# Kernel optimization log

Hardware: AMD Instinct MI355X
Metric: run time of the kernel (lower is better)

The kernel has to match this reference:

```python
import jax, jax.numpy as jnp
import numpy as np

N, C, K, KEIG, B, NG, H = 32768, 128, 5, 128, 64, 512, 4
E = 524288
EPS = 1e-5


def setup_inputs() -> dict:
    key = jax.random.key(0)
    ks = iter(jax.random.split(key, 40))
    def nrm(shape, scale):
        return jax.random.normal(next(ks), shape, jnp.float32) * scale
    s = 1.0 / np.sqrt(C)
    return dict(
        x=nrm((N, C), 1.0),
        U=nrm((N, KEIG), 1.0 / np.sqrt(N)),
        Lambda=jax.random.uniform(next(ks), (KEIG,), jnp.float32, 0.0, 2.0),
        lambda_max=jnp.full((1,), 2.0, jnp.float32),
        w_spa1=nrm((C, C), s), b_spa1=jnp.zeros((C,), jnp.float32),
        w_spa2=nrm((C, C), s), b_spa2=jnp.zeros((C,), jnp.float32),
        w_spe1=nrm((C, C), s), b_spe1=jnp.zeros((C,), jnp.float32),
        w_spe2=nrm((C, C), s), b_spe2=jnp.zeros((C,), jnp.float32),
        cheb_w=nrm((K, C, C), s), cheb_b=jnp.zeros((C,), jnp.float32),
        gamma=jnp.ones((1,), jnp.float32),
        w_proj=nrm((C, C), s),
        w_qkv=nrm((C, 3 * C), s), b_qkv=jnp.zeros((3 * C,), jnp.float32),
        w_out=nrm((C, C), s), b_out=jnp.zeros((C,), jnp.float32),
        mlp_w1=nrm((C, 2 * C), s), mlp_b1=jnp.zeros((2 * C,), jnp.float32),
        mlp_w2=nrm((2 * C, C), 1.0 / np.sqrt(2 * C)), mlp_b2=jnp.zeros((C,), jnp.float32),
        bn1_w=jnp.ones((C,), jnp.float32), bn1_b=jnp.zeros((C,), jnp.float32),
        bn2_w=jnp.ones((C,), jnp.float32), bn2_b=jnp.zeros((C,), jnp.float32),
        bn3_w=jnp.ones((C,), jnp.float32), bn3_b=jnp.zeros((C,), jnp.float32),
        edge_index=jax.random.randint(next(ks), (2, E), 0, N, jnp.int64) if jax.config.jax_enable_x64 else jax.random.randint(next(ks), (2, E), 0, N, jnp.int32),
        batch=jnp.repeat(jnp.arange(B), NG),  # 64 graphs of 512 nodes each
    )


def _mlp2(h, w1, b1, w2, b2):
    return jnp.maximum(h @ w1 + b1, 0.0) @ w2 + b2


def _bn(h, w, b):
    # train-mode BatchNorm1d over node dim (biased variance), GPSConv default norm
    mu = h.mean(0)
    var = jnp.mean((h - mu) ** 2, 0)
    return (h - mu) * jax.lax.rsqrt(var + EPS) * w + b


def _cheb(x, src, dst, lam, Ws, bias):
    # L_hat = (2/lambda_max) * (I - D^{-1/2} A D^{-1/2}) - I ; sym normalization
    deg = jax.ops.segment_sum(jnp.ones_like(src, x.dtype), src, num_segments=N)
    dis = jnp.where(deg > 0, 1.0 / jnp.sqrt(deg), 0.0)
    w = dis[src] * dis[dst]  # [E]
    scale = 2.0 / lam
    def lhat(v):
        agg = jax.ops.segment_sum(w[:, None] * v[src], dst, num_segments=N)
        return (scale - 1.0) * v - scale * agg
    Tx0 = x
    out = Tx0 @ Ws[0]
    Tx1 = lhat(Tx0)
    out = out + Tx1 @ Ws[1]
    for k in range(2, K):
        Tx2 = 2.0 * lhat(Tx1) - Tx0
        out = out + Tx2 @ Ws[k]
        Tx0, Tx1 = Tx1, Tx2
    return out + bias


def _mha(xd, w_qkv, b_qkv, w_out, b_out):
    Bq, n, _ = xd.shape
    dh = C // H
    qkv = xd @ w_qkv + b_qkv  # [B,n,3C]
    q, k, v = jnp.split(qkv, 3, axis=-1)
    heads = lambda t: t.reshape(Bq, n, H, dh).transpose(0, 2, 1, 3)
    q, k, v = heads(q), heads(k), heads(v)
    a = jax.nn.softmax(jnp.einsum('bhqd,bhkd->bhqk', q, k) / np.sqrt(dh), axis=-1)
    o = jnp.einsum('bhqk,bhkd->bhqd', a, v).transpose(0, 2, 1, 3).reshape(Bq, n, C)
    return o @ w_out + b_out


def reference(x, U, Lambda, lambda_max,
              w_spa1, b_spa1, w_spa2, b_spa2,
              w_spe1, b_spe1, w_spe2, b_spe2,
              cheb_w, cheb_b, gamma, w_proj,
              w_qkv, b_qkv, w_out, b_out,
              mlp_w1, mlp_b1, mlp_w2, mlp_b2,
              bn1_w, bn1_b, bn2_w, bn2_b, bn3_w, bn3_b,
              edge_index, batch):
    src, dst = edge_index[0], edge_index[1]
    lam = lambda_max[0]
    # ---- SpectralLocalNN (GPSConv local conv branch) ----
    x_sp = _mlp2(x, w_spa1, b_spa1, w_spa2, b_spa2)
    out_local = _cheb(x_sp, src, dst, lam, cheb_w, cheb_b)
    x_spec = _mlp2(x, w_spe1, b_spe1, w_spe2, b_spe2)
    h_proj = x_spec @ w_proj
    s_lam = jnp.exp(-gamma[0] * Lambda ** 2)  # [k_eig]
    out_spectral = U @ (s_lam[:, None] * (U.T @ h_proj))
    h1 = _bn(out_local + out_spectral + x, bn1_w, bn1_b)
    # ---- global attention branch (equal-size graphs -> dense reshape) ----
    xd = x.reshape(B, NG, C)
    h2 = _mha(xd, w_qkv, b_qkv, w_out, b_out).reshape(N, C)
    h2 = _bn(h2 + x, bn2_w, bn2_b)
    # ---- combine + MLP ----
    out = h1 + h2
    out = out + _mlp2(out, mlp_w1, mlp_b1, mlp_w2, mlp_b2)
    return _bn(out, bn3_w, bn3_b)
```

## Files before the change

### kernel.cpp

```cpp
#include <hip/hip_runtime.h>

typedef short bf16x8 __attribute__((ext_vector_type(8)));
typedef short bf16x4 __attribute__((ext_vector_type(4)));
typedef float f32x4 __attribute__((ext_vector_type(4)));

#define DEVI __device__ __forceinline__

constexpr int N   = 32768;
constexpr int C   = 128;
constexpr int E   = 524288;
constexpr float EPSV = 1e-5f;
constexpr int UT_BLOCKS = 128;
constexpr int HB  = 64;
constexpr int EPB = E / HB;
constexpr float QSCALE = 0.17677669529663687f * 1.4426950408889634f;

DEVI float bf2f(ushort u){ return __uint_as_float(((uint)u) << 16); }
DEVI ushort f2bf(float f){
  uint u = __float_as_uint(f);
  return (ushort)((u + 0x7fffu + ((u >> 16) & 1u)) >> 16);
}
DEVI uint cvtpk(float lo, float hi){
  uint r;
  asm("v_cvt_pk_bf16_f32 %0, %1, %2" : "=v"(r) : "v"(lo), "v"(hi));
  return r;
}
DEVI float fexp2(float x){
  float r;
  asm("v_exp_f32 %0, %1" : "=v"(r) : "v"(x));
  return r;
}
DEVI float sane(float v){ if (!(v == v)) return 0.f; return fminf(fmaxf(v, -1e30f), 1e30f); }
DEVI bool mode_fp32(const uint* lmraw){ return (lmraw[0] & 0xffffu) == 0u; }

constexpr int CSZ[28] = {128,1,16384,128,16384,128,16384,128,16384,128,81920,128,
                         1,16384,49152,384,16384,128,32768,256,32768,128,
                         128,128,128,128,128,128};
constexpr int COF[28] = {0,128,192,16576,16704,33088,33216,49600,49728,66112,
                         66240,148160,148288,148352,164736,213888,214272,230656,
                         230784,263552,263808,296576,296704,296832,296960,297088,
                         297216,297344};
constexpr int CAN_SMALL_TOTAL = 297472;

constexpr int WT_SPA1 = 0;
constexpr int WT_SPA2 = 16384;
constexpr int WT_SPE1 = 32768;
constexpr int WT_SPE2 = 49152;
constexpr int WT_PROJ = 65536;
constexpr int WT_CHEB = 81920;
constexpr int WT_QKV  = 163840;
constexpr int WT_WOUT = 212992;
constexpr int WT_MLP1 = 229376;
constexpr int WT_MLP2 = 262144;
constexpr int WT_TOTAL = 294912;

struct CvtArgs { const void* src[28]; };

DEVI ushort cvt_elem(const void* p, int j, bool f32){
  return f32 ? f2bf(((const float*)p)[j]) : ((const ushort*)p)[j];
}

__global__ __launch_bounds__(256) void prep_all(CvtArgs a,
    const void* __restrict__ xs, const void* __restrict__ Us,
    ushort* __restrict__ canx, ushort* __restrict__ canu,
    ushort* __restrict__ cs, ushort* __restrict__ wt,
    int* __restrict__ zp, const uint* __restrict__ lmraw)
{
  bool f32 = mode_fp32(lmraw);
  int b = blockIdx.x, tid = threadIdx.x;
  if (b < 8192) {
    size_t e = ((size_t)b * 256 + tid) * 4;
    bool isU = e >= (size_t)N * C;
    size_t off = isU ? e - (size_t)N * C : e;
    const void* src = isU ? Us : xs;
    ushort* dst = isU ? canu : canx;
    ushort4 o;
    if (f32) {
      float4 v = *(const float4*)((const float*)src + off);
      o.x = f2bf(v.x); o.y = f2bf(v.y); o.z = f2bf(v.z); o.w = f2bf(v.w);
    } else {
      o = *(const ushort4*)((const ushort*)src + off);
    }
    *(ushort4*)(dst + off) = o;
  } else if (b < 9354) {
    int idx = (b - 8192) * 256 + tid;
    #pragma unroll 1
    for (int s = 0; s < 28; s++) {
      if (idx < CSZ[s]) { cs[COF[s] + idx] = cvt_elem(a.src[s], idx, f32); return; }
      idx -= CSZ[s];
    }
  } else if (b < 10506) {
    int i = (b - 9354) * 256 + tid;
    if (i < 81920) {
      int m = i >> 14, r = i & 16383; int k = r >> 7, n = r & 127;
      const void* src = m==0?a.src[2] : m==1?a.src[4] : m==2?a.src[6] : m==3?a.src[8] : a.src[13];
      wt[m*16384 + n*128 + k] = cvt_elem(src, r, f32);
    } else if (i < 163840) {
      int j = i - 81920; int m = j >> 14, r = j & 16383; int k = r >> 7, n = r & 127;
      wt[WT_CHEB + n*640 + m*128 + k] = cvt_elem(a.src[10], j, f32);
    } else if (i < 212992) {
      int j = i - 163840; int k = j / 384, n = j % 384;
      wt[WT_QKV + n*128 + k] = cvt_elem(a.src[14], j, f32);
    } else if (i < 229376) {
      int j = i - 212992; int k = j >> 7, n = j & 127;
      wt[WT_WOUT + n*128 + k] = cvt_elem(a.src[16], j, f32);
    } else if (i < 262144) {
      int j = i - 229376; int k = j >> 8, n = j & 255;
      wt[WT_MLP1 + n*128 + k] = cvt_elem(a.src[18], j, f32);
    } else if (i < WT_TOTAL) {
      int j = i - 262144; int k = j >> 7, n = j & 127;
      wt[WT_MLP2 + n*256 + k] = cvt_elem(a.src[20], j, f32);
    }
  } else {
    int i = (b - 10506) * 256 + tid;
    if (i < 6144) zp[i] = 0;
  }
}

__global__ __launch_bounds__(1024) void hist_lds(const int* __restrict__ ei,
    int* __restrict__ cei, ushort* __restrict__ part)
{
  __shared__ uint hist[N / 2];
  int t = threadIdx.x;
  int b = blockIdx.x;
  bool i64 = ((ei[1] | ei[3] | ei[5] | ei[7]) == 0);
  size_t j0 = (size_t)b * EPB;
  #pragma unroll
  for (int i = t; i < N / 2; i += 1024) hist[i] = 0u;
  __syncthreads();
  for (int k = t; k < EPB; k += 1024) {
    size_t j = j0 + k;
    int v = (i64 ? ei[2 * j] : ei[j]) & (N - 1);
    cei[j] = v;
    atomicAdd(&hist[v >> 1], 1u << ((v & 1) * 16));
  }
  __syncthreads();
  uint* po = (uint*)(part + (size_t)b * N);
  for (int i = t; i < N / 2; i += 1024) po[i] = hist[i];
}

__global__ __launch_bounds__(256) void reduce_cnt(const ushort* __restrict__ part,
    int* __restrict__ cdt, float* __restrict__ dis)
{
  int d = blockIdx.x * 256 + threadIdx.x;
  int s = 0, tt = 0;
  #pragma unroll 8
  for (int b = 0; b < HB; b++) s  += part[(size_t)b * N + d];
  #pragma unroll 8
  for (int b = 0; b < HB; b++) tt += part[(size_t)(HB + b) * N + d];
  cdt[d] = tt;
  dis[d] = s > 0 ? rsqrtf((float)s) : 0.f;
}

__global__ __launch_bounds__(1024) void scan_kernel(const int* __restrict__ cnt,
                                                    int* __restrict__ row_ptr)
{
  __shared__ int sums[1024];
  int t = threadIdx.x;
  int loc[32]; int s = 0;
  int base = t * 32;
  #pragma unroll
  for (int i = 0; i < 32; i++) { loc[i] = s; s += cnt[base + i]; }
  sums[t] = s;
  __syncthreads();
  for (int off = 1; off < 1024; off <<= 1) {
    int v = (t >= off) ? sums[t - off] : 0;
    __syncthreads();
    sums[t] += v;
    __syncthreads();
  }
  int pre = (t == 0) ? 0 : sums[t - 1];
  #pragma unroll
  for (int i = 0; i < 32; i++) row_ptr[base + i] = pre + loc[i];
}

__global__ __launch_bounds__(256) void off_kernel(const int* __restrict__ rp,
    const ushort* __restrict__ part, int* __restrict__ off2)
{
  int d = blockIdx.x * 256 + threadIdx.x;
  int run = rp[d];
  #pragma unroll 8
  for (int b = 0; b < HB; b++) {
    off2[(size_t)b * N + d] = run;
    run += part[(size_t)(HB + b) * N + d];
  }
}

__global__ __launch_bounds__(1024) void edge_scatter(const int* __restrict__ cei,
    const int* __restrict__ off2, const float* __restrict__ dis,
    int2* __restrict__ ep)
{
  __shared__ int base[N];
  int t = threadIdx.x;
  int b = blockIdx.x;
  for (int i = t; i < N; i += 1024) base[i] = off2[(size_t)b * N + i];
  __syncthreads();
  size_t e0 = (size_t)b * EPB;
  for (int k = t; k < EPB; k += 1024) {
    size_t e = e0 + k;
    int s = cei[e], d = cei[e + E];
    int slot = atomicAdd(&base[d], 1);
    int2 v; v.x = s; v.y = __float_as_int(dis[s] * dis[d]);
    ep[slot] = v;
  }
}

template<int K, int COLS, bool RELU, int OMODE, bool BIAS, bool RES, int ASTR, int OSTR, bool QSC, bool STATS>
__global__ __launch_bounds__(256) void gemm_lds(
    const ushort* __restrict__ A, const ushort* __restrict__ WT,
    const ushort* __restrict__ bias, const ushort* __restrict__ res,
    void* __restrict__ outp, float* __restrict__ gstats)
{
  constexpr int NSEG = COLS / 128;
  constexpr int NKC = K / 128;
  constexpr int BP = 136;
  __shared__ ushort Bs[128 * BP];
  __shared__ float ls[STATS ? 256 : 1];
  int tid = threadIdx.x;
  int lane = tid & 63, wave = tid >> 6;
  int quad = lane >> 4, l16 = lane & 15;
  int seg = (NSEG > 1) ? (blockIdx.x % NSEG) : 0;
  int rb  = (NSEG > 1) ? (blockIdx.x / NSEG) : blockIdx.x;
  int row0 = rb * 64 + wave * 16;
  const ushort* wseg = WT + (size_t)(seg * 128) * K;

  f32x4 acc[8];
  #pragma unroll
  for (int nt = 0; nt < 8; nt++) acc[nt] = (f32x4){0.f, 0.f, 0.f, 0.f};

  for (int kc = 0; kc < NKC; kc++) {
    if (kc) __syncthreads();
    #pragma unroll
    for (int i = tid; i < 2048; i += 256) {
      int col = i >> 4, ko = (i & 15) * 8;
      *(bf16x8*)&Bs[col * BP + ko] =
          *(const bf16x8*)(wseg + (size_t)col * K + kc * 128 + ko);
    }
    __syncthreads();
    bf16x8 a[4];
    const ushort* ap = A + (size_t)(row0 + l16) * ASTR + kc * 128 + quad * 8;
    #pragma unroll
    for (int kk = 0; kk < 4; kk++) a[kk] = *(const bf16x8*)(ap + kk * 32);
    #pragma unroll
    for (int kk = 0; kk < 4; kk++) {
      #pragma unroll
      for (int nt = 0; nt < 8; nt++) {
        bf16x8 b = *(const bf16x8*)(&Bs[(nt * 16 + l16) * BP + kk * 32 + quad * 8]);
        acc[nt] = __builtin_amdgcn_mfma_f32_16x16x32_bf16(a[kk], b, acc[nt], 0, 0, 0);
      }
    }
  }

  if (STATS) {
    if (tid < 256) ls[tid] = 0.f;
    __syncthreads();
  }

  #pragma unroll
  for (int nt = 0; nt < 8; nt++) {
    int col = seg * 128 + nt * 16 + l16;
    float bv = 0.f;
    if (BIAS) bv = bf2f(bias[col]);
    float cs_ = 0.f, cs2 = 0.f;
    #pragma unroll
    for (int r = 0; r < 4; r++) {
      int row = row0 + quad * 4 + r;
      size_t oi = (size_t)row * OSTR + col;
      float v = acc[nt][r] + bv;
      if (RES) v += bf2f(res[(size_t)row * COLS + col]);
      if (RELU) v = fmaxf(v, 0.f);
      if (QSC && col < 128) v *= QSCALE;
      float nv;
      if (OMODE == 0)      { ((ushort*)outp)[oi] = f2bf(v); nv = v; }
      else if (OMODE == 1) { ((float*)outp)[oi] = v; nv = v; }
      else                 { float* fo = (float*)outp + oi; nv = *fo + v; *fo = nv; }
      if (STATS) { float sv = sane(nv); cs_ += sv; cs2 += sv * sv; }
    }
    if (STATS) { atomicAdd(&ls[col], cs_); atomicAdd(&ls[128 + col], cs2); }
  }

  if (STATS) {
    __syncthreads();
    float* gs = gstats + (blockIdx.x & 7) * 256;
    if (tid < 128) {
      atomicAdd(&gs[tid], ls[tid]);
      atomicAdd(&gs[128 + tid], ls[128 + tid]);
    }
  }
}

template<bool THIRD, int OSTR>
__global__ __launch_bounds__(256) void gemm_chain(
    const ushort* __restrict__ A,
    const ushort* __restrict__ W1, const ushort* __restrict__ B1,
    const ushort* __restrict__ W2, const ushort* __restrict__ B2,
    const ushort* __restrict__ W3,
    ushort* __restrict__ outp)
{
  constexpr int BP = 136;
  __shared__ ushort Bs[128 * BP];
  __shared__ ushort Ts[64 * BP];
  int tid = threadIdx.x;
  int lane = tid & 63, wave = tid >> 6;
  int quad = lane >> 4, l16 = lane & 15;
  int row0 = blockIdx.x * 64 + wave * 16;
  int lw = wave * 16;

  for (int i = tid; i < 2048; i += 256) {
    int col = i >> 4, ko = (i & 15) * 8;
    *(bf16x8*)&Bs[col * BP + ko] = *(const bf16x8*)(W1 + (size_t)col * 128 + ko);
  }
  __syncthreads();
  bf16x8 a[4];
  {
    const ushort* ap = A + (size_t)(row0 + l16) * 128 + quad * 8;
    #pragma unroll
    for (int kk = 0; kk < 4; kk++) a[kk] = *(const bf16x8*)(ap + kk * 32);
  }
  f32x4 acc[8];
  #pragma unroll
  for (int nt = 0; nt < 8; nt++) acc[nt] = (f32x4){0.f, 0.f, 0.f, 0.f};
  #pragma unroll
  for (int kk = 0; kk < 4; kk++)
    #pragma unroll
    for (int nt = 0; nt < 8; nt++) {
      bf16x8 b = *(const bf16x8*)(&Bs[(nt * 16 + l16) * BP + kk * 32 + quad * 8]);
      acc[nt] = __builtin_amdgcn_mfma_f32_16x16x32_bf16(a[kk], b, acc[nt], 0, 0, 0);
    }
  #pragma unroll
  for (int nt = 0; nt < 8; nt++) {
    int col = nt * 16 + l16;
    float bv = bf2f(B1[col]);
    #pragma unroll
    for (int r = 0; r < 4; r++)
      Ts[(lw + quad * 4 + r) * BP + col] = f2bf(fmaxf(acc[nt][r] + bv, 0.f));
  }
  __syncthreads();

  for (int i = tid; i < 2048; i += 256) {
    int col = i >> 4, ko = (i & 15) * 8;
    *(bf16x8*)&Bs[col * BP + ko] = *(const bf16x8*)(W2 + (size_t)col * 128 + ko);
  }
  #pragma unroll
  for (int kk = 0; kk < 4; kk++)
    a[kk] = *(const bf16x8*)(&Ts[(lw + l16) * BP + kk * 32 + quad * 8]);
  __syncthreads();
  #pragma unroll
  for (int nt = 0; nt < 8; nt++) acc[nt] = (f32x4){0.f, 0.f, 0.f, 0.f};
  #pragma unroll
  for (int kk = 0; kk < 4; kk++)
    #pragma unroll
    for (int nt = 0; nt < 8; nt++) {
      bf16x8 b = *(const bf16x8*)(&Bs[(nt * 16 + l16) * BP + kk * 32 + quad * 8]);
      acc[nt] = __builtin_amdgcn_mfma_f32_16x16x32_bf16(a[kk], b, acc[nt], 0, 0, 0);
    }

  if (!THIRD) {
    #pragma unroll
    for (int nt = 0; nt < 8; nt++) {
      int col = nt * 16 + l16;
      float bv = bf2f(B2[col]);
      #pragma unroll
      for (int r = 0; r < 4; r++)
        outp[(size_t)(row0 + quad * 4 + r) * OSTR + col] = f2bf(acc[nt][r] + bv);
    }
    return;
  }

  __syncthreads();
  #pragma unroll
  for (int nt = 0; nt < 8; nt++) {
    int col = nt * 16 + l16;
    float bv = bf2f(B2[col]);
    #pragma unroll
    for (int r = 0; r < 4; r++)
      Ts[(lw + quad * 4 + r) * BP + col] = f2bf(acc[nt][r] + bv);
  }
  __syncthreads();
  for (int i = tid; i < 2048; i += 256) {
    int col = i >> 4, ko = (i & 15) * 8;
    *(bf16x8*)&Bs[col * BP + ko] = *(const bf16x8*)(W3 + (size_t)col * 128 + ko);
  }
  #pragma unroll
  for (int kk = 0; kk < 4; kk++)
    a[kk] = *(const bf16x8*)(&Ts[(lw + l16) * BP + kk * 32 + quad * 8]);
  __syncthreads();
  #pragma unroll
  for (int nt = 0; nt < 8; nt++) acc[nt] = (f32x4){0.f, 0.f, 0.f, 0.f};
  #pragma unroll
  for (int kk = 0; kk < 4; kk++)
    #pragma unroll
    for (int nt = 0; nt < 8; nt++) {
      bf16x8 b = *(const bf16x8*)(&Bs[(nt * 16 + l16) * BP + kk * 32 + quad * 8]);
      acc[nt] = __builtin_amdgcn_mfma_f32_16x16x32_bf16(a[kk], b, acc[nt], 0, 0, 0);
    }
  #pragma unroll
  for (int nt = 0; nt < 8; nt++) {
    int col = nt * 16 + l16;
    #pragma unroll
    for (int r = 0; r < 4; r++)
      outp[(size_t)(row0 + quad * 4 + r) * OSTR + col] = f2bf(acc[nt][r]);
  }
}

__global__ __launch_bounds__(256) void gemm_mlp(
    const ushort* __restrict__ A,
    const ushort* __restrict__ W1, const ushort* __restrict__ B1,
    const ushort* __restrict__ W2, const ushort* __restrict__ B2,
    const ushort* __restrict__ res, float* __restrict__ outp,
    float* __restrict__ gstats)
{
  constexpr int BP = 136;
  constexpr int HP = 264;
  __shared__ ushort Bs[128 * BP];
  __shared__ ushort Hs[64 * HP];
  __shared__ float ls[256];
  int tid = threadIdx.x;
  int lane = tid & 63, wave = tid >> 6;
  int quad = lane >> 4, l16 = lane & 15;
  int row0 = blockIdx.x * 64 + wave * 16;
  int lw = wave * 16;

  bf16x8 a[4];
  {
    const ushort* ap = A + (size_t)(row0 + l16) * 128 + quad * 8;
    #pragma unroll
    for (int kk = 0; kk < 4; kk++) a[kk] = *(const bf16x8*)(ap + kk * 32);
  }

  for (int seg = 0; seg < 2; seg++) {
    if (seg) __syncthreads();
    for (int i = tid; i < 2048; i += 256) {
      int col = i >> 4, ko = (i & 15) * 8;
      *(bf16x8*)&Bs[col * BP + ko] =
          *(const bf16x8*)(W1 + (size_t)(seg * 128 + col) * 128 + ko);
    }
    __syncthreads();
    f32x4 acc[8];
    #pragma unroll
    for (int nt = 0; nt < 8; nt++) acc[nt] = (f32x4){0.f, 0.f, 0.f, 0.f};
    #pragma unroll
    for (int kk = 0; kk < 4; kk++)
      #pragma unroll
      for (int nt = 0; nt < 8; nt++) {
        bf16x8 b = *(const bf16x8*)(&Bs[(nt * 16 + l16) * BP + kk * 32 + quad * 8]);
        acc[nt] = __builtin_amdgcn_mfma_f32_16x16x32_bf16(a[kk], b, acc[nt], 0, 0, 0);
      }
    #pragma unroll
    for (int nt = 0; nt < 8; nt++) {
      int col = seg * 128 + nt * 16 + l16;
      float bv = bf2f(B1[col]);
      #pragma unroll
      for (int r = 0; r < 4; r++)
        Hs[(lw + quad * 4 + r) * HP + col] = f2bf(fmaxf(acc[nt][r] + bv, 0.f));
    }
  }
  __syncthreads();
  if (tid < 256) ls[tid] = 0.f;

  f32x4 acc2[8];
  #pragma unroll
  for (int nt = 0; nt < 8; nt++) acc2[nt] = (f32x4){0.f, 0.f, 0.f, 0.f};
  for (int kc = 0; kc < 2; kc++) {
    if (kc) __syncthreads();
    for (int i = tid; i < 2048; i += 256) {
      int col = i >> 4, ko = (i & 15) * 8;
      *(bf16x8*)&Bs[col * BP + ko] =
          *(const bf16x8*)(W2 + (size_t)col * 256 + kc * 128 + ko);
    }
    bf16x8 a2[4];
    #pragma unroll
    for (int kk = 0; kk < 4; kk++)
      a2[kk] = *(const bf16x8*)(&Hs[(lw + l16) * HP + kc * 128 + kk * 32 + quad * 8]);
    __syncthreads();
    #pragma unroll
    for (int kk = 0; kk < 4; kk++)
      #pragma unroll
      for (int nt = 0; nt < 8; nt++) {
        bf16x8 b = *(const bf16x8*)(&Bs[(nt * 16 + l16) * BP + kk * 32 + quad * 8]);
        acc2[nt] = __builtin_amdgcn_mfma_f32_16x16x32_bf16(a2[kk], b, acc2[nt], 0, 0, 0);
      }
  }

  #pragma unroll
  for (int nt = 0; nt < 8; nt++) {
    int col = nt * 16 + l16;
    float bv = bf2f(B2[col]);
    float cs_ = 0.f, cs2 = 0.f;
    #pragma unroll
    for (int r = 0; r < 4; r++) {
      int row = row0 + quad * 4 + r;
      float v = acc2[nt][r] + bv + bf2f(res[(size_t)row * 128 + col]);
      outp[(size_t)row * 128 + col] = v;
      float sv = sane(v); cs_ += sv; cs2 += sv * sv;
    }
    atomicAdd(&ls[col], cs_); atomicAdd(&ls[128 + col], cs2);
  }
  __syncthreads();
  float* gs = gstats + (blockIdx.x & 7) * 256;
  if (tid < 128) {
    atomicAdd(&gs[tid], ls[tid]);
    atomicAdd(&gs[128 + tid], ls[128 + tid]);
  }
}

__global__ __launch_bounds__(256) void spmm_cheb(
    const int* __restrict__ row_ptr, const int2* __restrict__ ep,
    const ushort* __restrict__ v,
    const ushort* __restrict__ txprev, ushort* __restrict__ txout,
    const ushort* __restrict__ lambda_max, int first, int str)
{
  int wave = threadIdx.x >> 6, lane = threadIdx.x & 63;
  int sub = lane >> 4, l16 = lane & 15;
  int d = blockIdx.x * 4 + wave;
  float lm = bf2f(lambda_max[0]);
  float scale = 2.f / lm;
  if (!(scale == scale) || fabsf(scale) > 1e6f) scale = 1.f;
  int beg = row_ptr[d];
  int end = (d == N - 1) ? E : row_ptr[d + 1];
  float acc[8] = {0.f,0.f,0.f,0.f,0.f,0.f,0.f,0.f};
  int j0 = beg + sub;
  int2 e2 = ep[j0 < end ? j0 : 0];
  for (int jb = beg; jb < end; jb += 4) {
    int jn = jb + 4 + sub;
    int2 en = ep[jn < end ? jn : 0];
    bool ok = (jb + sub) < end;
    int s = e2.x & (N - 1);
    float w = ok ? __int_as_float(e2.y) : 0.f;
    bf16x8 vv = *(const bf16x8*)(v + (size_t)s * str + l16 * 8);
    #pragma unroll
    for (int i = 0; i < 8; i++) acc[i] += w * bf2f((ushort)vv[i]);
    e2 = en;
  }
  #pragma unroll
  for (int i = 0; i < 8; i++) {
    acc[i] += __shfl_xor(acc[i], 16);
    acc[i] += __shfl_xor(acc[i], 32);
  }
  if (sub == 0) {
    bf16x8 vd = *(const bf16x8*)(v + (size_t)d * str + l16 * 8);
    bf16x8 tp;
    if (!first) tp = *(const bf16x8*)(txprev + (size_t)d * str + l16 * 8);
    bf16x8 ov;
    #pragma unroll
    for (int i = 0; i < 8; i++) {
      float r = (scale - 1.f) * bf2f((ushort)vd[i]) - scale * acc[i];
      if (!first) r = 2.f * r - bf2f((ushort)tp[i]);
      ov[i] = (short)f2bf(r);
    }
    *(bf16x8*)(txout + (size_t)d * str + l16 * 8) = ov;
  }
}

__global__ __launch_bounds__(256) void ut_mfma(const ushort* __restrict__ U,
    const ushort* __restrict__ hp, float* __restrict__ parts)
{
  constexpr int RP = 40;
  __shared__ ushort Ut[128 * RP];
  __shared__ ushort Ht[128 * RP];
  int t = threadIdx.x;
  int lane = t & 63, wave = t >> 6;
  int quad = lane >> 4, l16 = lane & 15;

  f32x4 acc[2][8];
  #pragma unroll
  for (int a = 0; a < 2; a++)
    #pragma unroll
    for (int ct = 0; ct < 8; ct++) acc[a][ct] = (f32x4){0.f, 0.f, 0.f, 0.f};

  for (int ch = 0; ch < 8; ch++) {
    int n0 = blockIdx.x * 256 + ch * 32;
    __syncthreads();
    for (int i = t; i < 2048; i += 256) {
      int r2 = i >> 7, c = i & 127;
      uint u0 = U [(size_t)(n0 + r2 * 2) * 128 + c];
      uint u1 = U [(size_t)(n0 + r2 * 2 + 1) * 128 + c];
      *(uint*)&Ut[c * RP + r2 * 2] = (u0 & 0xffffu) | (u1 << 16);
      uint h0 = hp[(size_t)(n0 + r2 * 2) * 128 + c];
      uint h1 = hp[(size_t)(n0 + r2 * 2 + 1) * 128 + c];
      *(uint*)&Ht[c * RP + r2 * 2] = (h0 & 0xffffu) | (h1 << 16);
    }
    __syncthreads();
    bf16x8 bfr[8];
    #pragma unroll
    for (int ct = 0; ct < 8; ct++)
      bfr[ct] = *(const bf16x8*)(&Ht[(ct * 16 + l16) * RP + quad * 8]);
    #pragma unroll
    for (int a = 0; a < 2; a++) {
      int kt = wave * 2 + a;
      bf16x8 af = *(const bf16x8*)(&Ut[(kt * 16 + l16) * RP + quad * 8]);
      #pragma unroll
      for (int ct = 0; ct < 8; ct++)
        acc[a][ct] = __builtin_amdgcn_mfma_f32_16x16x32_bf16(af, bfr[ct], acc[a][ct], 0, 0, 0);
    }
  }

  float* po = parts + (size_t)blockIdx.x * 16384;
  #pragma unroll
  for (int a = 0; a < 2; a++) {
    int kt = wave * 2 + a;
    #pragma unroll
    for (int ct = 0; ct < 8; ct++)
      #pragma unroll
      for (int r = 0; r < 4; r++)
        po[(kt * 16 + quad * 4 + r) * 128 + ct * 16 + l16] = acc[a][ct][r];
  }
}

__global__ __launch_bounds__(256) void reduce_mt(const float* __restrict__ parts,
    const ushort* __restrict__ Lambda, const ushort* __restrict__ gamma,
    ushort* __restrict__ MT)
{
  int e = blockIdx.x * 256 + threadIdx.x;
  int keig = e >> 7, c = e & 127;
  float s = 0.f;
  for (int p = 0; p < UT_BLOCKS; p++) s += parts[(size_t)p * 16384 + e];
  float g = bf2f(gamma[0]);
  float lam = bf2f(Lambda[keig]);
  float sl = __expf(-g * lam * lam);
  MT[c * 128 + keig] = f2bf(sl * s);
}

__global__ __launch_bounds__(256) void bn_apply(const float* __restrict__ h,
    const float* __restrict__ st, const ushort* __restrict__ gw,
    const ushort* __restrict__ gb, const ushort* __restrict__ add,
    void* __restrict__ out, const uint* __restrict__ lmraw, int final_out)
{
  __shared__ float sk[128], sb[128];
  int tid = threadIdx.x;
  if (tid < 128) {
    float s = 0.f, s2 = 0.f;
    #pragma unroll
    for (int rr = 0; rr < 8; rr++) {
      s  += st[rr * 256 + tid];
      s2 += st[rr * 256 + 128 + tid];
    }
    float mu  = s * (1.f / 32768.f);
    float var = fmaxf(s2 * (1.f / 32768.f) - mu * mu, 0.f);
    float k = rsqrtf(var + EPSV) * bf2f(gw[tid]);
    sk[tid] = k;
    sb[tid] = bf2f(gb[tid]) - mu * k;
  }
  __syncthreads();
  size_t e = ((size_t)blockIdx.x * 256 + tid) * 4;
  int c0 = (int)(e & 127);
  float4 hv = *(const float4*)(h + e);
  float xv[4] = {sane(hv.x), sane(hv.y), sane(hv.z), sane(hv.w)};
  float addv[4] = {0.f, 0.f, 0.f, 0.f};
  if (add) {
    ushort4 av = *(const ushort4*)(add + e);
    addv[0] = bf2f(av.x); addv[1] = bf2f(av.y);
    addv[2] = bf2f(av.z); addv[3] = bf2f(av.w);
  }
  float r[4];
  #pragma unroll
  for (int j = 0; j < 4; j++) {
    int c = c0 + j;
    r[j] = xv[j] * sk[c] + sb[c] + addv[j];
  }
  if (final_out && mode_fp32(lmraw)) {
    float4 o4; o4.x = r[0]; o4.y = r[1]; o4.z = r[2]; o4.w = r[3];
    *(float4*)((float*)out + e) = o4;
  } else {
    ushort4 o;
    o.x = f2bf(r[0]); o.y = f2bf(r[1]); o.z = f2bf(r[2]); o.w = f2bf(r[3]);
    *(ushort4*)((ushort*)out + e) = o;
  }
}

__global__ __launch_bounds__(512) void attn_mfma(const ushort* __restrict__ qkv,
                                                 ushort* __restrict__ attn)
{
  constexpr int VP = 516;
  constexpr int KP = 40;
  __shared__ ushort Kt[512 * KP];
  __shared__ ushort Vt[32 * VP];
  int b = blockIdx.x;
  int g = b >> 3, hh = (b >> 1) & 3, half = b & 1;
  int lane = threadIdx.x & 63, wave = threadIdx.x >> 6;
  int quad = lane >> 4, l16 = lane & 15;
  const ushort* base = qkv + (size_t)g * 512 * 384;

  for (int i = threadIdx.x; i < 512 * 4; i += 512) {
    int key = i >> 2, c8 = (i & 3) * 8;
    *(bf16x8*)&Kt[key * KP + c8] =
        *(const bf16x8*)(base + (size_t)key * 384 + 128 + hh * 32 + c8);
  }
  for (int i = threadIdx.x; i < 256 * 8; i += 512) {
    int kp = i >> 3, d4 = (i & 7) * 4;
    const ushort* va = base + (size_t)(2 * kp) * 384 + 256 + hh * 32 + d4;
    ushort4 a = *(const ushort4*)va;
    ushort4 c = *(const ushort4*)(va + 384);
    *(uint*)&Vt[(d4 + 0) * VP + 2 * kp] = (uint)a.x | ((uint)c.x << 16);
    *(uint*)&Vt[(d4 + 1) * VP + 2 * kp] = (uint)a.y | ((uint)c.y << 16);
    *(uint*)&Vt[(d4 + 2) * VP + 2 * kp] = (uint)a.z | ((uint)c.z << 16);
    *(uint*)&Vt[(d4 + 3) * VP + 2 * kp] = (uint)a.w | ((uint)c.w << 16);
  }
  __syncthreads();

  int q0 = half * 256 + wave * 32;
  bf16x8 qf[2];
  #pragma unroll
  for (int i = 0; i < 2; i++)
    qf[i] = *(const bf16x8*)(base + (size_t)(q0 + i * 16 + l16) * 384 + hh * 32 + quad * 8);

  f32x4 O[2][2];
  #pragma unroll
  for (int dt = 0; dt < 2; dt++)
    #pragma unroll
    for (int i = 0; i < 2; i++) O[dt][i] = (f32x4){0.f, 0.f, 0.f, 0.f};
  float lsum[2] = {0.f, 0.f};

  union PU { uint u[4]; bf16x8 v; };
  union VU { uint2 a[2]; bf16x8 v; };

  for (int kt2 = 0; kt2 < 16; kt2++) {
    int k0 = kt2 * 32;
    bf16x8 kfA = *(const bf16x8*)&Kt[(k0 + l16) * KP + quad * 8];
    bf16x8 kfB = *(const bf16x8*)&Kt[(k0 + 16 + l16) * KP + quad * 8];
    PU pw[2];
    #pragma unroll
    for (int i = 0; i < 2; i++) {
      f32x4 sA = __builtin_amdgcn_mfma_f32_16x16x32_bf16(kfA, qf[i], (f32x4){0.f,0.f,0.f,0.f}, 0, 0, 0);
      f32x4 sB = __builtin_amdgcn_mfma_f32_16x16x32_bf16(kfB, qf[i], (f32x4){0.f,0.f,0.f,0.f}, 0, 0, 0);
      float p0 = fexp2(fminf(sA[0], 86.5f));
      float p1 = fexp2(fminf(sA[1], 86.5f));
      float p2 = fexp2(fminf(sA[2], 86.5f));
      float p3 = fexp2(fminf(sA[3], 86.5f));
      float p4 = fexp2(fminf(sB[0], 86.5f));
      float p5 = fexp2(fminf(sB[1], 86.5f));
      float p6 = fexp2(fminf(sB[2], 86.5f));
      float p7 = fexp2(fminf(sB[3], 86.5f));
      lsum[i] += ((p0 + p1) + (p2 + p3)) + ((p4 + p5) + (p6 + p7));
      pw[i].u[0] = cvtpk(p0, p1); pw[i].u[1] = cvtpk(p2, p3);
      pw[i].u[2] = cvtpk(p4, p5); pw[i].u[3] = cvtpk(p6, p7);
    }
    #pragma unroll
    for (int dt = 0; dt < 2; dt++) {
      int drow = (dt * 16 + l16) * VP;
      VU vu;
      vu.a[0] = *(const uint2*)&Vt[drow + k0 + quad * 4];
      vu.a[1] = *(const uint2*)&Vt[drow + k0 + 16 + quad * 4];
      #pragma unroll
      for (int i = 0; i < 2; i++)
        O[dt][i] = __builtin_amdgcn_mfma_f32_16x16x32_bf16(vu.v, pw[i].v, O[dt][i], 0, 0, 0);
    }
  }

  #pragma unroll
  for (int i = 0; i < 2; i++) {
    float l = lsum[i];
    l += __shfl_xor(l, 16);
    l += __shfl_xor(l, 32);
    lsum[i] = 1.f / l;
  }

  #pragma unroll
  for (int i = 0; i < 2; i++) {
    size_t node = (size_t)g * 512 + q0 + i * 16 + l16;
    #pragma unroll
    for (int dt = 0; dt < 2; dt++) {
      uint2 o;
      o.x = cvtpk(O[dt][i][0] * lsum[i], O[dt][i][1] * lsum[i]);
      o.y = cvtpk(O[dt][i][2] * lsum[i], O[dt][i][3] * lsum[i]);
      *(uint2*)(attn + node * 128 + hh * 32 + dt * 16 + quad * 4) = o;
    }
  }
}

constexpr size_t KB = 1024;
constexpr size_t MB = 1048576;
constexpr size_t OFF_WT    = 0;
constexpr size_t OFF_CDT   = 576 * KB;
constexpr size_t OFF_RP    = 704 * KB;
constexpr size_t OFF_DIS   = 832 * KB;
constexpr size_t OFF_MT    = 960 * KB;
constexpr size_t OFF_STATS = 1024 * KB;
constexpr size_t OFF_CEI   = 6  * MB;
constexpr size_t OFF_EP    = 10 * MB;
constexpr size_t OFF_CANX  = 14 * MB;
constexpr size_t OFF_CANU  = 22 * MB;
constexpr size_t OFF_CANS  = 30 * MB;
constexpr size_t OFF_F1    = 31 * MB;
constexpr size_t OFF_HPROJ = 39 * MB;
constexpr size_t OFF_TBIG  = 47 * MB;
constexpr size_t OFF_PARTH = OFF_TBIG;
constexpr size_t OFF_OFF2  = OFF_TBIG + 8 * MB;
constexpr size_t OFF_PARTS = 87 * MB;

extern "C" void kernel_launch(void* const* d_in, const int* in_sizes, int n_in,
                              void* d_out, int out_size, void* d_ws, size_t ws_size,
                              hipStream_t stream) {
  (void)in_sizes; (void)n_in; (void)out_size; (void)ws_size;
  const uint* lmraw = (const uint*)d_in[3];
  const int*  ei    = (const int*)d_in[30];

  char* W = (char*)d_ws;
  ushort* wt    = (ushort*)(W + OFF_WT);
  int*    cdt   = (int*)(W + OFF_CDT);
  int*    rp    = (int*)(W + OFF_RP);
  float*  dis   = (float*)(W + OFF_DIS);
  ushort* MT    = (ushort*)(W + OFF_MT);
  float*  stats = (float*)(W + OFF_STATS);
  int*    cei   = (int*)(W + OFF_CEI);
  int2*   ep    = (int2*)(W + OFF_EP);
  ushort* part  = (ushort*)(W + OFF_PARTH);
  int*    off2  = (int*)(W + OFF_OFF2);
  ushort* canx  = (ushort*)(W + OFF_CANX);
  ushort* canu  = (ushort*)(W + OFF_CANU);
  ushort* cs    = (ushort*)(W + OFF_CANS);
  float*  F1    = (float*)(W + OFF_F1);
  ushort* hproj = (ushort*)(W + OFF_HPROJ);
  ushort* Tbig  = (ushort*)(W + OFF_TBIG);
  ushort* qkvb  = (ushort*)(W + OFF_TBIG);
  float*  parts = (float*)(W + OFF_PARTS);
  ushort* attnb = (ushort*)(W + OFF_PARTS);
  ushort* h1    = (ushort*)(W + OFF_CANU);
  ushort* comb  = (ushort*)(W + OFF_CANX);

  const ushort* cLambda = cs + COF[0];
  const ushort* cLmx    = cs + COF[1];
  const ushort* cBspa1  = cs + COF[3];
  const ushort* cBspa2  = cs + COF[5];
  const ushort* cBspe1  = cs + COF[7];
  const ushort* cBspe2  = cs + COF[9];
  const ushort* cChebB  = cs + COF[11];
  const ushort* cGam    = cs + COF[12];
  const ushort* cBqkv   = cs + COF[15];
  const ushort* cBout   = cs + COF[17];
  const ushort* cMb1    = cs + COF[19];
  const ushort* cMb2    = cs + COF[21];
  const ushort* cBn1w   = cs + COF[22];
  const ushort* cBn1b   = cs + COF[23];
  const ushort* cBn2w   = cs + COF[24];
  const ushort* cBn2b   = cs + COF[25];
  const ushort* cBn3w   = cs + COF[26];
  const ushort* cBn3b   = cs + COF[27];

  const ushort* NUL = nullptr;
  float* NULF = nullptr;

  CvtArgs ca;
  ca.src[0]  = d_in[2];  ca.src[1]  = d_in[3];  ca.src[2]  = d_in[4];
  ca.src[3]  = d_in[5];  ca.src[4]  = d_in[6];  ca.src[5]  = d_in[7];
  ca.src[6]  = d_in[8];  ca.src[7]  = d_in[9];  ca.src[8]  = d_in[10];
  ca.src[9]  = d_in[11]; ca.src[10] = d_in[12]; ca.src[11] = d_in[13];
  ca.src[12] = d_in[14]; ca.src[13] = d_in[15]; ca.src[14] = d_in[16];
  ca.src[15] = d_in[17]; ca.src[16] = d_in[18]; ca.src[17] = d_in[19];
  ca.src[18] = d_in[20]; ca.src[19] = d_in[21]; ca.src[20] = d_in[22];
  ca.src[21] = d_in[23]; ca.src[22] = d_in[24]; ca.src[23] = d_in[25];
  ca.src[24] = d_in[26]; ca.src[25] = d_in[27]; ca.src[26] = d_in[28];
  ca.src[27] = d_in[29];
  prep_all<<<10530, 256, 0, stream>>>(ca, d_in[0], d_in[1], canx, canu, cs, wt,
                                      (int*)(W + OFF_STATS), lmraw);

  hist_lds<<<2 * HB, 1024, 0, stream>>>(ei, cei, part);
  reduce_cnt<<<N / 256, 256, 0, stream>>>(part, cdt, dis);
  scan_kernel<<<1, 1024, 0, stream>>>(cdt, rp);
  off_kernel<<<N / 256, 256, 0, stream>>>(rp, part, off2);
  edge_scatter<<<HB, 1024, 0, stream>>>(cei, off2, dis, ep);

  dim3 g1(512), g3(1536), bb(256);
  gemm_chain<false, 640><<<g1, bb, 0, stream>>>(canx, wt + WT_SPA1, cBspa1,
      wt + WT_SPA2, cBspa2, NUL, Tbig);
  gemm_chain<true, 128><<<g1, bb, 0, stream>>>(canx, wt + WT_SPE1, cBspe1,
      wt + WT_SPE2, cBspe2, wt + WT_PROJ, hproj);

  ut_mfma<<<UT_BLOCKS, 256, 0, stream>>>(canu, hproj, parts);
  reduce_mt<<<64, 256, 0, stream>>>(parts, cLambda, cGam, MT);

  spmm_cheb<<<N / 4, 256, 0, stream>>>(rp, ep, Tbig,       NUL,        Tbig + 128, cLmx, 1, 640);
  spmm_cheb<<<N / 4, 256, 0, stream>>>(rp, ep, Tbig + 128, Tbig,       Tbig + 256, cLmx, 0, 640);
  spmm_cheb<<<N / 4, 256, 0, stream>>>(rp, ep, Tbig + 256, Tbig + 128, Tbig + 384, cLmx, 0, 640);
  spmm_cheb<<<N / 4, 256, 0, stream>>>(rp, ep, Tbig + 384, Tbig + 256, Tbig + 512, cLmx, 0, 640);
  gemm_lds<640,128,false,1,true ,false,640,128,false,false><<<g1, bb, 0, stream>>>(Tbig, wt + WT_CHEB, cChebB, NUL, F1, NULF);

  gemm_lds<128,128,false,2,false,true ,128,128,false,true ><<<g1, bb, 0, stream>>>(canu, MT, NUL, canx, F1, stats);
  bn_apply<<<(N * C) / 1024, 256, 0, stream>>>(F1, stats, cBn1w, cBn1b, NUL, h1, lmraw, 0);

  gemm_lds<128,384,false,0,true ,false,128,384,true ,false><<<g3, bb, 0, stream>>>(canx, wt + WT_QKV, cBqkv, NUL, qkvb, NULF);
  attn_mfma<<<512, 512, 0, stream>>>(qkvb, attnb);
  gemm_lds<128,128,false,1,true ,true ,128,128,false,true ><<<g1, bb, 0, stream>>>(attnb, wt + WT_WOUT, cBout, canx, F1, stats + 2048);
  bn_apply<<<(N * C) / 1024, 256, 0, stream>>>(F1, stats + 2048, cBn2w, cBn2b, h1, comb, lmraw, 0);

  gemm_mlp<<<g1, bb, 0, stream>>>(comb, wt + WT_MLP1, cMb1, wt + WT_MLP2, cMb2, comb, F1, stats + 4096);
  bn_apply<<<(N * C) / 1024, 256, 0, stream>>>(F1, stats + 4096, cBn3w, cBn3b, NUL, d_out, lmraw, 1);
}
```

Measured before the change: 504.9 us.

## Fuse BN1/BN2 apply, add dedicated QKV GEMM, deepen SpMM prefetch

Merges the two separate BatchNorm apply passes into one kernel that reads both fp32 pre-norm buffers and writes the combined bf16 sum. This removes the write and re-read of the intermediate h1 buffer and one kernel launch, at the cost of a second fp32 buffer in the workspace. It also replaces the templated QKV GEMM with a kernel that keeps the A tile in registers and loops over the three 128-column weight segments. The Chebyshev SpMM now prefetches edges two iterations ahead and gathers the feature row one iteration ahead, to hide gather latency at the cost of extra registers.

```diff
diff --git a/kernel.cpp b/kernel.cpp
--- a/kernel.cpp
+++ b/kernel.cpp
@@ -289,6 +289,56 @@
   }
 }
 
+__global__ __launch_bounds__(256) void gemm_qkv(
+    const ushort* __restrict__ A, const ushort* __restrict__ WT,
+    const ushort* __restrict__ bias, ushort* __restrict__ outp)
+{
+  constexpr int BP = 136;
+  __shared__ ushort Bs[128 * BP];
+  int tid = threadIdx.x;
+  int lane = tid & 63, wave = tid >> 6;
+  int quad = lane >> 4, l16 = lane & 15;
+  int row0 = blockIdx.x * 64 + wave * 16;
+  bf16x8 a[4];
+  {
+    const ushort* ap = A + (size_t)(row0 + l16) * 128 + quad * 8;
+    #pragma unroll
+    for (int kk = 0; kk < 4; kk++) a[kk] = *(const bf16x8*)(ap + kk * 32);
+  }
+
+  #pragma unroll 1
+  for (int seg = 0; seg < 3; seg++) {
+    if (seg) __syncthreads();
+    for (int i = tid; i < 2048; i += 256) {
+      int col = i >> 4, ko = (i & 15) * 8;
+      *(bf16x8*)&Bs[col * BP + ko] =
+          *(const bf16x8*)(WT + (size_t)(seg * 128 + col) * 128 + ko);
+    }
+    __syncthreads();
+    f32x4 acc[8];
+    #pragma unroll
+    for (int nt = 0; nt < 8; nt++) acc[nt] = (f32x4){0.f, 0.f, 0.f, 0.f};
+    #pragma unroll
+    for (int kk = 0; kk < 4; kk++)
+      #pragma unroll
+      for (int nt = 0; nt < 8; nt++) {
+        bf16x8 b = *(const bf16x8*)(&Bs[(nt * 16 + l16) * BP + kk * 32 + quad * 8]);
+        acc[nt] = __builtin_amdgcn_mfma_f32_16x16x32_bf16(a[kk], b, acc[nt], 0, 0, 0);
+      }
+    #pragma unroll
+    for (int nt = 0; nt < 8; nt++) {
+      int col = seg * 128 + nt * 16 + l16;
+      float bv = bf2f(bias[col]);
+      #pragma unroll
+      for (int r = 0; r < 4; r++) {
+        float v = acc[nt][r] + bv;
+        if (seg == 0) v *= QSCALE;
+        outp[(size_t)(row0 + quad * 4 + r) * 384 + col] = f2bf(v);
+      }
+    }
+  }
+}
+
 template<bool THIRD, int OSTR>
 __global__ __launch_bounds__(256) void gemm_chain(
     const ushort* __restrict__ A,
@@ -520,17 +570,18 @@
   int end = (d == N - 1) ? E : row_ptr[d + 1];
   float acc[8] = {0.f,0.f,0.f,0.f,0.f,0.f,0.f,0.f};
   int j0 = beg + sub;
-  int2 e2 = ep[j0 < end ? j0 : 0];
+  int2 eA = ep[j0 < end ? j0 : 0];
+  int2 eB = ep[(j0 + 4) < end ? (j0 + 4) : 0];
+  bf16x8 vA = *(const bf16x8*)(v + (size_t)(eA.x & (N - 1)) * str + l16 * 8);
   for (int jb = beg; jb < end; jb += 4) {
-    int jn = jb + 4 + sub;
-    int2 en = ep[jn < end ? jn : 0];
+    int jc = jb + 8 + sub;
+    int2 eC = ep[jc < end ? jc : 0];
+    bf16x8 vB = *(const bf16x8*)(v + (size_t)(eB.x & (N - 1)) * str + l16 * 8);
     bool ok = (jb + sub) < end;
-    int s = e2.x & (N - 1);
-    float w = ok ? __int_as_float(e2.y) : 0.f;
-    bf16x8 vv = *(const bf16x8*)(v + (size_t)s * str + l16 * 8);
-    #pragma unroll
-    for (int i = 0; i < 8; i++) acc[i] += w * bf2f((ushort)vv[i]);
-    e2 = en;
+    float w = ok ? __int_as_float(eA.y) : 0.f;
+    #pragma unroll
+    for (int i = 0; i < 8; i++) acc[i] += w * bf2f((ushort)vA[i]);
+    eA = eB; eB = eC; vA = vB;
   }
   #pragma unroll
   for (int i = 0; i < 8; i++) {
@@ -666,6 +717,50 @@
     o.x = f2bf(r[0]); o.y = f2bf(r[1]); o.z = f2bf(r[2]); o.w = f2bf(r[3]);
     *(ushort4*)((ushort*)out + e) = o;
   }
+}
+
+__global__ __launch_bounds__(256) void bn12_apply(
+    const float* __restrict__ ha, const float* __restrict__ hb,
+    const float* __restrict__ st1, const float* __restrict__ st2,
+    const ushort* __restrict__ w1, const ushort* __restrict__ b1,
+    const ushort* __restrict__ w2, const ushort* __restrict__ b2,
+    ushort* __restrict__ comb)
+{
+  __shared__ float k1[128], o1[128], k2[128], o2[128];
+  int tid = threadIdx.x;
+  if (tid < 128) {
+    float s = 0.f, s2 = 0.f, t = 0.f, t2 = 0.f;
+    #pragma unroll
+    for (int rr = 0; rr < 8; rr++) {
+      s  += st1[rr * 256 + tid];  s2 += st1[rr * 256 + 128 + tid];
+      t  += st2[rr * 256 + tid];  t2 += st2[rr * 256 + 128 + tid];
+    }
+    float mu  = s * (1.f / 32768.f);
+    float var = fmaxf(s2 * (1.f / 32768.f) - mu * mu, 0.f);
+    float k = rsqrtf(var + EPSV) * bf2f(w1[tid]);
+    k1[tid] = k; o1[tid] = bf2f(b1[tid]) - mu * k;
+    mu  = t * (1.f / 32768.f);
+    var = fmaxf(t2 * (1.f / 32768.f) - mu * mu, 0.f);
+    k = rsqrtf(var + EPSV) * bf2f(w2[tid]);
+    k2[tid] = k; o2[tid] = bf2f(b2[tid]) - mu * k;
+  }
+  __syncthreads();
+  size_t e = ((size_t)blockIdx.x * 256 + tid) * 4;
+  int c0 = (int)(e & 127);
+  float4 av = *(const float4*)(ha + e);
+  float4 bv = *(const float4*)(hb + e);
+  float xa[4] = {sane(av.x), sane(av.y), sane(av.z), sane(av.w)};
+  float xb[4] = {sane(bv.x), sane(bv.y), sane(bv.z), sane(bv.w)};
+  ushort4 o;
+  ushort r_[4];
+  #pragma unroll
+  for (int j = 0; j < 4; j++) {
+    int c = c0 + j;
+    float h1v = bf2f(f2bf(xa[j] * k1[c] + o1[c]));
+    r_[j] = f2bf(xb[j] * k2[c] + o2[c] + h1v);
+  }
+  o.x = r_[0]; o.y = r_[1]; o.z = r_[2]; o.w = r_[3];
+  *(ushort4*)(comb + e) = o;
 }
 
 __global__ __launch_bounds__(512) void attn_mfma(const ushort* __restrict__ qkv,
@@ -786,6 +881,7 @@
 constexpr size_t OFF_TBIG  = 47 * MB;
 constexpr size_t OFF_PARTH = OFF_TBIG;
 constexpr size_t OFF_OFF2  = OFF_TBIG + 8 * MB;
+constexpr size_t OFF_F1B   = 71 * MB;
 constexpr size_t OFF_PARTS = 87 * MB;
 
 extern "C" void kernel_launch(void* const* d_in, const int* in_sizes, int n_in,
@@ -810,12 +906,12 @@
   ushort* canu  = (ushort*)(W + OFF_CANU);
   ushort* cs    = (ushort*)(W + OFF_CANS);
   float*  F1    = (float*)(W + OFF_F1);
+  float*  F1B   = (float*)(W + OFF_F1B);
   ushort* hproj = (ushort*)(W + OFF_HPROJ);
   ushort* Tbig  = (ushort*)(W + OFF_TBIG);
   ushort* qkvb  = (ushort*)(W + OFF_TBIG);
   float*  parts = (float*)(W + OFF_PARTS);
   ushort* attnb = (ushort*)(W + OFF_PARTS);
-  ushort* h1    = (ushort*)(W + OFF_CANU);
   ushort* comb  = (ushort*)(W + OFF_CANX);
 
   const ushort* cLambda = cs + COF[0];
@@ -860,7 +956,7 @@
   off_kernel<<<N / 256, 256, 0, stream>>>(rp, part, off2);
   edge_scatter<<<HB, 1024, 0, stream>>>(cei, off2, dis, ep);
 
-  dim3 g1(512), g3(1536), bb(256);
+  dim3 g1(512), bb(256);
   gemm_chain<false, 640><<<g1, bb, 0, stream>>>(canx, wt + WT_SPA1, cBspa1,
       wt + WT_SPA2, cBspa2, NUL, Tbig);
   gemm_chain<true, 128><<<g1, bb, 0, stream>>>(canx, wt + WT_SPE1, cBspe1,
@@ -876,12 +972,13 @@
   gemm_lds<640,128,false,1,true ,false,640,128,false,false><<<g1, bb, 0, stream>>>(Tbig, wt + WT_CHEB, cChebB, NUL, F1, NULF);
 
   gemm_lds<128,128,false,2,false,true ,128,128,false,true ><<<g1, bb, 0, stream>>>(canu, MT, NUL, canx, F1, stats);
-  bn_apply<<<(N * C) / 1024, 256, 0, stream>>>(F1, stats, cBn1w, cBn1b, NUL, h1, lmraw, 0);
-
-  gemm_lds<128,384,false,0,true ,false,128,384,true ,false><<<g3, bb, 0, stream>>>(canx, wt + WT_QKV, cBqkv, NUL, qkvb, NULF);
+
+  gemm_qkv<<<g1, bb, 0, stream>>>(canx, wt + WT_QKV, cBqkv, qkvb);
   attn_mfma<<<512, 512, 0, stream>>>(qkvb, attnb);
-  gemm_lds<128,128,false,1,true ,true ,128,128,false,true ><<<g1, bb, 0, stream>>>(attnb, wt + WT_WOUT, cBout, canx, F1, stats + 2048);
-  bn_apply<<<(N * C) / 1024, 256, 0, stream>>>(F1, stats + 2048, cBn2w, cBn2b, h1, comb, lmraw, 0);
+  gemm_lds<128,128,false,1,true ,true ,128,128,false,true ><<<g1, bb, 0, stream>>>(attnb, wt + WT_WOUT, cBout, canx, F1B, stats + 2048);
+
+  bn12_apply<<<(N * C) / 1024, 256, 0, stream>>>(F1, F1B, stats, stats + 2048,
+      cBn1w, cBn1b, cBn2w, cBn2b, comb);
 
   gemm_mlp<<<g1, bb, 0, stream>>>(comb, wt + WT_MLP1, cMb1, wt + WT_MLP2, cMb2, comb, F1, stats + 4096);
   bn_apply<<<(N * C) / 1024, 256, 0, stream>>>(F1, stats + 4096, cBn3w, cBn3b, NUL, d_out, lmraw, 1);
```

Result: faster. 483.0 us (-4.3%).
